# Kernel tuning notes

Hardware: AMD Instinct MI355X
Metric: run time of the kernel (lower is better)

Reference implementation:

```python
import jax, jax.numpy as jnp
import numpy as np

LATENT = 2000
N_GROUPS = 10000  # loci_count // window_size
KERNEL = 20       # window_size * 2; per-group input length is 1 so out length == KERNEL
BATCH = 128
EPS = 1e-5
SLOPE = 0.1


def setup_inputs() -> dict:
    key = jax.random.key(0)
    k1, k2, k3, k4, k5 = jax.random.split(key, 5)
    return {
        "z": jax.random.normal(k1, (BATCH, LATENT), dtype=jnp.float32),
        "W_fc": jax.random.normal(k2, (N_GROUPS, LATENT), dtype=jnp.float32) * 0.02,
        "b_fc": jax.random.normal(k3, (N_GROUPS,), dtype=jnp.float32) * 0.02,
        "gamma": jnp.ones((N_GROUPS,), dtype=jnp.float32),
        "beta": jnp.zeros((N_GROUPS,), dtype=jnp.float32),
        "conv_w": jax.random.normal(k4, (N_GROUPS, KERNEL), dtype=jnp.float32) * 0.1,
        "conv_b": jax.random.normal(k5, (N_GROUPS,), dtype=jnp.float32) * 0.02,
    }


def reference(z, W_fc, b_fc, gamma, beta, conv_w, conv_b):
    # Linear: (B, L) @ (L, G) -> (B, G)
    h = jnp.einsum("bl,gl->bg", z, W_fc) + b_fc
    # BatchNorm1d (training mode: biased batch statistics, eps=1e-5)
    mean = jnp.mean(h, axis=0)
    var = jnp.mean(jnp.square(h - mean), axis=0)
    h = (h - mean) * jax.lax.rsqrt(var + EPS) * gamma + beta
    h = jnp.where(h >= 0, h, SLOPE * h)  # LeakyReLU(0.1)
    # Grouped ConvTranspose1d with per-group input length 1 degenerates to
    # an outer product per channel: y[b,g,k] = h[b,g]*w[g,k] + b[g]
    y = h[:, :, None] * conv_w[None, :, :] + conv_b[None, :, None]  # (B, G, K)
    y = jnp.where(y >= 0, y, SLOPE * y)  # LeakyReLU(0.1)
    out = jax.nn.sigmoid(y.reshape(z.shape[0], N_GROUPS * KERNEL))
    return out
```

## Files before the change

kernel.cpp:

```cpp
#include <hip/hip_runtime.h>
#include <hip/hip_bf16.h>
#include <stdint.h>

#define BATCH 128
#define LAT   2000
#define NG    10000
#define KW    20
#define OUTW  (NG * KW)
#define EPSV  1e-5f

#define GT    64
#define BK    64
#define KSPL  4

typedef __bf16 bf16x8 __attribute__((ext_vector_type(8)));
typedef float  f32x4  __attribute__((ext_vector_type(4)));

__device__ __forceinline__ ushort f2bf(float f) {
  uint32_t u = __builtin_bit_cast(uint32_t, f);
  u = (u + 0x7FFFu + ((u >> 16) & 1u)) >> 16;
  return (ushort)u;
}

__device__ __forceinline__ int4 pack8(const float* p) {
  float4 f0 = *(const float4*)p;
  float4 f1 = *(const float4*)(p + 4);
  int4 v;
  v.x = (int)((uint32_t)f2bf(f0.x) | ((uint32_t)f2bf(f0.y) << 16));
  v.y = (int)((uint32_t)f2bf(f0.z) | ((uint32_t)f2bf(f0.w) << 16));
  v.z = (int)((uint32_t)f2bf(f1.x) | ((uint32_t)f2bf(f1.y) << 16));
  v.w = (int)((uint32_t)f2bf(f1.z) | ((uint32_t)f2bf(f1.w) << 16));
  return v;
}

__global__ __launch_bounds__(256, 4) void gemm_splitk_kernel(
    const float* __restrict__ zp, const float* __restrict__ wp,
    float* __restrict__ hp) {
  const int tid = threadIdx.x;
  const int g0  = blockIdx.x * GT;
  const int s   = blockIdx.y;
  const int kbase = s * 512;
  const int klen  = (s < 3) ? 512 : (LAT - 3 * 512);

  __shared__ ushort As[GT * BK];
  __shared__ ushort Bs[BATCH * BK];

  const int lane = tid & 63;
  const int w    = tid >> 6;
  const int wm   = w & 1;
  const int wn   = w >> 1;
  const int q    = lane >> 4;
  const int cl   = lane & 15;

  f32x4 acc[2][4];
  const f32x4 vzero = {0.f, 0.f, 0.f, 0.f};
#pragma unroll
  for (int i = 0; i < 2; ++i)
#pragma unroll
    for (int j = 0; j < 4; ++j) acc[i][j] = vzero;

  for (int it = 0; it < 8; ++it) {
    const int k0 = it * BK;
    __syncthreads();

#pragma unroll
    for (int i = 0; i < 2; ++i) {
      int c = i * 256 + tid;
      int r = c >> 3, sc = c & 7;
      int lk = k0 + sc * 8;
      int g  = g0 + r;
      int4 v = make_int4(0, 0, 0, 0);
      if (lk < klen && g < NG)
        v = pack8(wp + (size_t)g * LAT + kbase + lk);
      *(int4*)&As[r * BK + ((sc ^ (r & 7)) << 3)] = v;
    }
#pragma unroll
    for (int i = 0; i < 4; ++i) {
      int c = i * 256 + tid;
      int r = c >> 3, sc = c & 7;
      int lk = k0 + sc * 8;
      int4 v = make_int4(0, 0, 0, 0);
      if (lk < klen)
        v = pack8(zp + (size_t)r * LAT + kbase + lk);
      *(int4*)&Bs[r * BK + ((sc ^ (r & 7)) << 3)] = v;
    }
    __syncthreads();

#pragma unroll
    for (int kk = 0; kk < 2; ++kk) {
      int sc = kk * 4 + q;
      bf16x8 af[2], bfr[4];
#pragma unroll
      for (int mt = 0; mt < 2; ++mt) {
        int ra = wm * 32 + mt * 16 + cl;
        af[mt] = *(const bf16x8*)&As[ra * BK + ((sc ^ (ra & 7)) << 3)];
      }
#pragma unroll
      for (int nt = 0; nt < 4; ++nt) {
        int rb = wn * 64 + nt * 16 + cl;
        bfr[nt] = *(const bf16x8*)&Bs[rb * BK + ((sc ^ (rb & 7)) << 3)];
      }
#pragma unroll
      for (int mt = 0; mt < 2; ++mt)
#pragma unroll
        for (int nt = 0; nt < 4; ++nt)
          acc[mt][nt] = __builtin_amdgcn_mfma_f32_16x16x32_bf16(
              af[mt], bfr[nt], acc[mt][nt], 0, 0, 0);
    }
  }

  float* base = hp + (size_t)s * NG * BATCH;
#pragma unroll
  for (int mt = 0; mt < 2; ++mt) {
#pragma unroll
    for (int r = 0; r < 4; ++r) {
      int g = g0 + wm * 32 + mt * 16 + q * 4 + r;
      if (g < NG) {
#pragma unroll
        for (int nt = 0; nt < 4; ++nt) {
          int b = wn * 64 + nt * 16 + cl;
          base[(size_t)g * BATCH + b] = acc[mt][nt][r];
        }
      }
    }
  }
}

__global__ __launch_bounds__(256, 4) void stats_kernel(
    const float* __restrict__ hp, const float* __restrict__ gammap,
    const float* __restrict__ betap, float* __restrict__ scalep,
    float* __restrict__ shiftp) {
  const int tid = threadIdx.x;
  const int g   = blockIdx.x * 8 + (tid >> 5);
  const int l32 = tid & 31;

  float4 hv = make_float4(0.f, 0.f, 0.f, 0.f);
#pragma unroll
  for (int s = 0; s < KSPL; ++s) {
    float4 v = *(const float4*)(hp + ((size_t)s * NG + g) * BATCH + l32 * 4);
    hv.x += v.x; hv.y += v.y; hv.z += v.z; hv.w += v.w;
  }
  float sm = hv.x + hv.y + hv.z + hv.w;
  float sq = hv.x * hv.x + hv.y * hv.y + hv.z * hv.z + hv.w * hv.w;
#pragma unroll
  for (int m = 1; m < 32; m <<= 1) {
    sm += __shfl_xor(sm, m);
    sq += __shfl_xor(sq, m);
  }
  if (l32 == 0) {
    float mean = sm * (1.f / 128.f);
    float var  = sq * (1.f / 128.f) - mean * mean;
    var = (var < 0.f) ? 0.f : var;
    float inv   = __builtin_amdgcn_rsqf(var + EPSV);
    float scale = inv * gammap[g];
    scalep[g] = scale;
    shiftp[g] = betap[g] - mean * scale;
  }
}

__global__ __launch_bounds__(256, 4) void expand_kernel(
    const float* __restrict__ hp, const float* __restrict__ scalep,
    const float* __restrict__ shiftp, const float* __restrict__ convwp,
    const float* __restrict__ convbp, float* __restrict__ out) {
  const int tid = threadIdx.x;
  const int g   = blockIdx.x * 8 + (tid >> 5);
  const int bc  = (tid & 31) * 4;

  float4 hv = make_float4(0.f, 0.f, 0.f, 0.f);
#pragma unroll
  for (int s = 0; s < KSPL; ++s) {
    float4 v = *(const float4*)(hp + ((size_t)s * NG + g) * BATCH + bc);
    hv.x += v.x; hv.y += v.y; hv.z += v.z; hv.w += v.w;
  }

  const float scale = scalep[g];
  const float shift = shiftp[g];
  const float cb    = convbp[g];
  float wv[KW];
  {
    const float4* pw = (const float4*)(convwp + (size_t)g * KW);
#pragma unroll
    for (int j = 0; j < 5; ++j) {
      float4 f = pw[j];
      wv[4 * j] = f.x; wv[4 * j + 1] = f.y;
      wv[4 * j + 2] = f.z; wv[4 * j + 3] = f.w;
    }
  }

  float hb[4] = {hv.x, hv.y, hv.z, hv.w};
#pragma unroll
  for (int i = 0; i < 4; ++i) {
    float h = hb[i] * scale + shift;
    h = fmaxf(h, h * 0.1f);
    float4 ov[5];
#pragma unroll
    for (int j = 0; j < 5; ++j) {
      float y0 = h * wv[4 * j]     + cb;
      float y1 = h * wv[4 * j + 1] + cb;
      float y2 = h * wv[4 * j + 2] + cb;
      float y3 = h * wv[4 * j + 3] + cb;
      y0 = fmaxf(y0, y0 * 0.1f);
      y1 = fmaxf(y1, y1 * 0.1f);
      y2 = fmaxf(y2, y2 * 0.1f);
      y3 = fmaxf(y3, y3 * 0.1f);
      ov[j].x = __builtin_amdgcn_rcpf(1.f + exp2f(y0 * -1.44269504f));
      ov[j].y = __builtin_amdgcn_rcpf(1.f + exp2f(y1 * -1.44269504f));
      ov[j].z = __builtin_amdgcn_rcpf(1.f + exp2f(y2 * -1.44269504f));
      ov[j].w = __builtin_amdgcn_rcpf(1.f + exp2f(y3 * -1.44269504f));
    }
    float4* po = (float4*)(out + (size_t)(bc + i) * OUTW + (size_t)g * KW);
#pragma unroll
    for (int j = 0; j < 5; ++j) po[j] = ov[j];
  }
}

__global__ __launch_bounds__(256, 2) void fused_decoder_kernel(
    const float* __restrict__ zp, const float* __restrict__ wp,
    const float* __restrict__ gammap, const float* __restrict__ betap,
    const float* __restrict__ convwp, const float* __restrict__ convbp,
    float* __restrict__ out) {
  const int tid = threadIdx.x;
  const int g0  = blockIdx.x * 32;

  __shared__ ushort As[BATCH * BK];
  __shared__ ushort Bs[32 * BK];
  __shared__ float statS[2][2][16];
  __shared__ float statQ[2][2][16];

  const int lane = tid & 63;
  const int w    = tid >> 6;
  const int wm   = w & 1;
  const int wn   = w >> 1;
  const int q    = lane >> 4;
  const int cl   = lane & 15;

  f32x4 acc[4];
  const f32x4 vzero = {0.f, 0.f, 0.f, 0.f};
#pragma unroll
  for (int i = 0; i < 4; ++i) acc[i] = vzero;

  for (int it = 0; it < 32; ++it) {
    const int k0 = it * BK;
    __syncthreads();
#pragma unroll
    for (int i = 0; i < 4; ++i) {
      int c = i * 256 + tid;
      int r = c >> 3, sc = c & 7;
      int gk = k0 + sc * 8;
      int4 v = make_int4(0, 0, 0, 0);
      if (gk < LAT) v = pack8(zp + (size_t)r * LAT + gk);
      *(int4*)&As[r * BK + ((sc ^ (r & 7)) << 3)] = v;
    }
    {
      int r = tid >> 3, sc = tid & 7;
      int g  = g0 + r;
      int gk = k0 + sc * 8;
      int4 v = make_int4(0, 0, 0, 0);
      if (gk < LAT && g < NG) v = pack8(wp + (size_t)g * LAT + gk);
      *(int4*)&Bs[r * BK + ((sc ^ (r & 7)) << 3)] = v;
    }
    __syncthreads();
#pragma unroll
    for (int kk = 0; kk < 2; ++kk) {
      int sc = kk * 4 + q;
      bf16x8 af[4], bfr;
#pragma unroll
      for (int mt = 0; mt < 4; ++mt) {
        int ra = wm * 64 + mt * 16 + cl;
        af[mt] = *(const bf16x8*)&As[ra * BK + ((sc ^ (ra & 7)) << 3)];
      }
      {
        int rb = wn * 16 + cl;
        bfr = *(const bf16x8*)&Bs[rb * BK + ((sc ^ (rb & 7)) << 3)];
      }
#pragma unroll
      for (int mt = 0; mt < 4; ++mt)
        acc[mt] = __builtin_amdgcn_mfma_f32_16x16x32_bf16(af[mt], bfr,
                                                          acc[mt], 0, 0, 0);
    }
  }

  float s = 0.f, ss = 0.f;
#pragma unroll
  for (int mt = 0; mt < 4; ++mt)
#pragma unroll
    for (int r = 0; r < 4; ++r) {
      float v = acc[mt][r];
      s += v; ss += v * v;
    }
  s += __shfl_xor(s, 16); ss += __shfl_xor(ss, 16);
  s += __shfl_xor(s, 32); ss += __shfl_xor(ss, 32);
  if (q == 0) { statS[wm][wn][cl] = s; statQ[wm][wn][cl] = ss; }
  __syncthreads();

  const int gcol = g0 + wn * 16 + cl;
  const int gc   = (gcol < NG) ? gcol : (NG - 1);
  float S = statS[0][wn][cl] + statS[1][wn][cl];
  float Q = statQ[0][wn][cl] + statQ[1][wn][cl];
  float mean = S * (1.f / 128.f);
  float var  = Q * (1.f / 128.f) - mean * mean;
  var = (var < 0.f) ? 0.f : var;
  float inv = __builtin_amdgcn_rsqf(var + EPSV);
  float ga = gammap[gc], be = betap[gc], cb = convbp[gc];
  float wv[KW];
  {
    const float4* pw = (const float4*)(convwp + (size_t)gc * KW);
#pragma unroll
    for (int j = 0; j < 5; ++j) {
      float4 f = pw[j];
      wv[4 * j] = f.x; wv[4 * j + 1] = f.y;
      wv[4 * j + 2] = f.z; wv[4 * j + 3] = f.w;
    }
  }
  float scale = inv * ga;
  float shift = be - mean * scale;
  const bool ok = (gcol < NG);
#pragma unroll
  for (int mt = 0; mt < 4; ++mt) {
#pragma unroll
    for (int r = 0; r < 4; ++r) {
      float h = acc[mt][r] * scale + shift;
      h = fmaxf(h, h * 0.1f);
      int b = wm * 64 + mt * 16 + q * 4 + r;
      float4 ov[5];
#pragma unroll
      for (int j = 0; j < 5; ++j) {
        float y0 = h * wv[4 * j]     + cb;
        float y1 = h * wv[4 * j + 1] + cb;
        float y2 = h * wv[4 * j + 2] + cb;
        float y3 = h * wv[4 * j + 3] + cb;
        y0 = fmaxf(y0, y0 * 0.1f);
        y1 = fmaxf(y1, y1 * 0.1f);
        y2 = fmaxf(y2, y2 * 0.1f);
        y3 = fmaxf(y3, y3 * 0.1f);
        ov[j].x = __builtin_amdgcn_rcpf(1.f + exp2f(y0 * -1.44269504f));
        ov[j].y = __builtin_amdgcn_rcpf(1.f + exp2f(y1 * -1.44269504f));
        ov[j].z = __builtin_amdgcn_rcpf(1.f + exp2f(y2 * -1.44269504f));
        ov[j].w = __builtin_amdgcn_rcpf(1.f + exp2f(y3 * -1.44269504f));
      }
      if (ok) {
        float4* po = (float4*)(out + (size_t)b * OUTW + (size_t)gcol * KW);
#pragma unroll
        for (int j = 0; j < 5; ++j) po[j] = ov[j];
      }
    }
  }
}

extern "C" void kernel_launch(void* const* d_in, const int* in_sizes, int n_in,
                              void* d_out, int out_size, void* d_ws, size_t ws_size,
                              hipStream_t stream) {
  const float* z     = (const float*)d_in[0];
  const float* W     = (const float*)d_in[1];
  const float* gamma = (const float*)d_in[3];
  const float* beta  = (const float*)d_in[4];
  const float* convw = (const float*)d_in[5];
  const float* convb = (const float*)d_in[6];
  float* out = (float*)d_out;

  const size_t hp_elems = (size_t)KSPL * NG * BATCH;
  const size_t need = (hp_elems + 2 * NG) * sizeof(float);

  if (ws_size >= need) {
    float* hp     = (float*)d_ws;
    float* scalep = hp + hp_elems;
    float* shiftp = scalep + NG;

    dim3 g1((NG + GT - 1) / GT, KSPL);
    gemm_splitk_kernel<<<g1, 256, 0, stream>>>(z, W, hp);
    stats_kernel<<<NG / 8, 256, 0, stream>>>(hp, gamma, beta, scalep, shiftp);
    expand_kernel<<<NG / 8, 256, 0, stream>>>(hp, scalep, shiftp, convw,
                                              convb, out);
  } else {
    fused_decoder_kernel<<<(NG + 31) / 32, 256, 0, stream>>>(
        z, W, gamma, beta, convw, convb, out);
  }
}
```

Measured before the change: 222.3 us.

## Fuse batchnorm stats and expand kernels with coalesced LDS-staged output writes

Result: faster. 206.2 us (-7.3%).

```diff
diff --git a/kernel.cpp b/kernel.cpp
--- a/kernel.cpp
+++ b/kernel.cpp
@@ -12,6 +12,9 @@
 #define GT    64
 #define BK    64
 #define KSPL  4
+
+#define EG        16
+#define HR_STRIDE 132
 
 typedef __bf16 bf16x8 __attribute__((ext_vector_type(8)));
 typedef float  f32x4  __attribute__((ext_vector_type(4)));
@@ -126,91 +129,92 @@
   }
 }
 
-__global__ __launch_bounds__(256, 4) void stats_kernel(
+__global__ __launch_bounds__(256, 4) void bn_expand_kernel(
     const float* __restrict__ hp, const float* __restrict__ gammap,
-    const float* __restrict__ betap, float* __restrict__ scalep,
-    float* __restrict__ shiftp) {
-  const int tid = threadIdx.x;
-  const int g   = blockIdx.x * 8 + (tid >> 5);
-  const int l32 = tid & 31;
-
-  float4 hv = make_float4(0.f, 0.f, 0.f, 0.f);
-#pragma unroll
-  for (int s = 0; s < KSPL; ++s) {
-    float4 v = *(const float4*)(hp + ((size_t)s * NG + g) * BATCH + l32 * 4);
-    hv.x += v.x; hv.y += v.y; hv.z += v.z; hv.w += v.w;
-  }
-  float sm = hv.x + hv.y + hv.z + hv.w;
-  float sq = hv.x * hv.x + hv.y * hv.y + hv.z * hv.z + hv.w * hv.w;
-#pragma unroll
-  for (int m = 1; m < 32; m <<= 1) {
-    sm += __shfl_xor(sm, m);
-    sq += __shfl_xor(sq, m);
-  }
-  if (l32 == 0) {
-    float mean = sm * (1.f / 128.f);
-    float var  = sq * (1.f / 128.f) - mean * mean;
-    var = (var < 0.f) ? 0.f : var;
-    float inv   = __builtin_amdgcn_rsqf(var + EPSV);
-    float scale = inv * gammap[g];
-    scalep[g] = scale;
-    shiftp[g] = betap[g] - mean * scale;
-  }
-}
-
-__global__ __launch_bounds__(256, 4) void expand_kernel(
-    const float* __restrict__ hp, const float* __restrict__ scalep,
-    const float* __restrict__ shiftp, const float* __restrict__ convwp,
+    const float* __restrict__ betap, const float* __restrict__ convwp,
     const float* __restrict__ convbp, float* __restrict__ out) {
   const int tid = threadIdx.x;
-  const int g   = blockIdx.x * 8 + (tid >> 5);
-  const int bc  = (tid & 31) * 4;
-
-  float4 hv = make_float4(0.f, 0.f, 0.f, 0.f);
-#pragma unroll
-  for (int s = 0; s < KSPL; ++s) {
-    float4 v = *(const float4*)(hp + ((size_t)s * NG + g) * BATCH + bc);
-    hv.x += v.x; hv.y += v.y; hv.z += v.z; hv.w += v.w;
-  }
-
-  const float scale = scalep[g];
-  const float shift = shiftp[g];
-  const float cb    = convbp[g];
-  float wv[KW];
-  {
-    const float4* pw = (const float4*)(convwp + (size_t)g * KW);
-#pragma unroll
-    for (int j = 0; j < 5; ++j) {
-      float4 f = pw[j];
-      wv[4 * j] = f.x; wv[4 * j + 1] = f.y;
-      wv[4 * j + 2] = f.z; wv[4 * j + 3] = f.w;
-    }
-  }
-
-  float hb[4] = {hv.x, hv.y, hv.z, hv.w};
-#pragma unroll
-  for (int i = 0; i < 4; ++i) {
-    float h = hb[i] * scale + shift;
-    h = fmaxf(h, h * 0.1f);
-    float4 ov[5];
-#pragma unroll
-    for (int j = 0; j < 5; ++j) {
-      float y0 = h * wv[4 * j]     + cb;
-      float y1 = h * wv[4 * j + 1] + cb;
-      float y2 = h * wv[4 * j + 2] + cb;
-      float y3 = h * wv[4 * j + 3] + cb;
-      y0 = fmaxf(y0, y0 * 0.1f);
-      y1 = fmaxf(y1, y1 * 0.1f);
-      y2 = fmaxf(y2, y2 * 0.1f);
-      y3 = fmaxf(y3, y3 * 0.1f);
-      ov[j].x = __builtin_amdgcn_rcpf(1.f + exp2f(y0 * -1.44269504f));
-      ov[j].y = __builtin_amdgcn_rcpf(1.f + exp2f(y1 * -1.44269504f));
-      ov[j].z = __builtin_amdgcn_rcpf(1.f + exp2f(y2 * -1.44269504f));
-      ov[j].w = __builtin_amdgcn_rcpf(1.f + exp2f(y3 * -1.44269504f));
-    }
-    float4* po = (float4*)(out + (size_t)(bc + i) * OUTW + (size_t)g * KW);
-#pragma unroll
-    for (int j = 0; j < 5; ++j) po[j] = ov[j];
+  const int g0  = blockIdx.x * EG;
+
+  __shared__ float  h_raw[EG * HR_STRIDE];
+  __shared__ float4 cw_s[EG * 5];
+  __shared__ float  cb_s[EG];
+  __shared__ float  scale_s[EG];
+  __shared__ float  shift_s[EG];
+
+  if (tid < EG * 5)
+    cw_s[tid] = *(const float4*)(convwp + (size_t)g0 * KW + tid * 4);
+  if (tid < EG) cb_s[tid] = convbp[g0 + tid];
+
+  float sm[2], sq[2];
+#pragma unroll
+  for (int half = 0; half < 2; ++half) {
+    const int idx = tid + half * 256;
+    const int gl  = idx >> 5;
+    const int bb  = (idx & 31) * 4;
+    float4 a = make_float4(0.f, 0.f, 0.f, 0.f);
+#pragma unroll
+    for (int s = 0; s < KSPL; ++s) {
+      const float4 v =
+          *(const float4*)(hp + ((size_t)s * NG + g0 + gl) * BATCH + bb);
+      a.x += v.x; a.y += v.y; a.z += v.z; a.w += v.w;
+    }
+    *(float4*)&h_raw[gl * HR_STRIDE + bb] = a;
+    sm[half] = a.x + a.y + a.z + a.w;
+    sq[half] = a.x * a.x + a.y * a.y + a.z * a.z + a.w * a.w;
+  }
+#pragma unroll
+  for (int m = 1; m < 32; m <<= 1) {
+    sm[0] += __shfl_xor(sm[0], m); sq[0] += __shfl_xor(sq[0], m);
+    sm[1] += __shfl_xor(sm[1], m); sq[1] += __shfl_xor(sq[1], m);
+  }
+  if ((tid & 31) == 0) {
+#pragma unroll
+    for (int half = 0; half < 2; ++half) {
+      const int gl = (tid >> 5) + half * 8;
+      float mean = sm[half] * (1.f / 128.f);
+      float var  = sq[half] * (1.f / 128.f) - mean * mean;
+      var = (var < 0.f) ? 0.f : var;
+      float inv   = __builtin_amdgcn_rsqf(var + EPSV);
+      float scale = inv * gammap[g0 + gl];
+      scale_s[gl] = scale;
+      shift_s[gl] = betap[g0 + gl] - mean * scale;
+    }
+  }
+  __syncthreads();
+
+  if (tid < 240) {
+    const int col4 = tid % 80;
+    const int r0   = tid / 80;
+    const int gl   = col4 / 5;
+    const float4 w4  = cw_s[col4];
+    const float  cb  = cb_s[gl];
+    const float  scl = scale_s[gl];
+    const float  sft = shift_s[gl];
+    const float* hsrc = &h_raw[gl * HR_STRIDE];
+    float* obase = out + (size_t)g0 * KW + (size_t)col4 * 4;
+    for (int j = 0; j < 43; ++j) {
+      const int row = j * 3 + r0;
+      if (row < BATCH) {
+        float h = hsrc[row];
+        h = fmaf(h, scl, sft);
+        h = fmaxf(h, h * 0.1f);
+        float y0 = fmaf(h, w4.x, cb);
+        float y1 = fmaf(h, w4.y, cb);
+        float y2 = fmaf(h, w4.z, cb);
+        float y3 = fmaf(h, w4.w, cb);
+        y0 = fmaxf(y0, y0 * 0.1f);
+        y1 = fmaxf(y1, y1 * 0.1f);
+        y2 = fmaxf(y2, y2 * 0.1f);
+        y3 = fmaxf(y3, y3 * 0.1f);
+        float4 ov;
+        ov.x = __builtin_amdgcn_rcpf(1.f + exp2f(y0 * -1.44269504f));
+        ov.y = __builtin_amdgcn_rcpf(1.f + exp2f(y1 * -1.44269504f));
+        ov.z = __builtin_amdgcn_rcpf(1.f + exp2f(y2 * -1.44269504f));
+        ov.w = __builtin_amdgcn_rcpf(1.f + exp2f(y3 * -1.44269504f));
+        *(float4*)(obase + (size_t)row * OUTW) = ov;
+      }
+    }
   }
 }
 
@@ -359,18 +363,14 @@
   float* out = (float*)d_out;
 
   const size_t hp_elems = (size_t)KSPL * NG * BATCH;
-  const size_t need = (hp_elems + 2 * NG) * sizeof(float);
+  const size_t need = hp_elems * sizeof(float);
 
   if (ws_size >= need) {
-    float* hp     = (float*)d_ws;
-    float* scalep = hp + hp_elems;
-    float* shiftp = scalep + NG;
-
+    float* hp = (float*)d_ws;
     dim3 g1((NG + GT - 1) / GT, KSPL);
     gemm_splitk_kernel<<<g1, 256, 0, stream>>>(z, W, hp);
-    stats_kernel<<<NG / 8, 256, 0, stream>>>(hp, gamma, beta, scalep, shiftp);
-    expand_kernel<<<NG / 8, 256, 0, stream>>>(hp, scalep, shiftp, convw,
-                                              convb, out);
+    bn_expand_kernel<<<NG / EG, 256, 0, stream>>>(hp, gamma, beta, convw,
+                                                  convb, out);
   } else {
     fused_decoder_kernel<<<(NG + 31) / 32, 256, 0, stream>>>(
         z, W, gamma, beta, convw, convb, out);
```
